# Kernel tuning notes

Hardware: AMD Instinct MI355X
Metric: run time of the kernel (lower is better)

## Reference

```python
import jax, jax.numpy as jnp
import numpy as np

B, S, E = 2, 2048, 2048
NH, NKV, HD = 32, 8, 64
GS = NH // NKV  # group size = 4
EPS = 1e-6
ROPE_THETA = 10000.0


def setup_inputs() -> dict:
    key = jax.random.key(0)
    ks = jax.random.split(key, 6)
    x = jax.random.normal(ks[0], (B, S, E), jnp.float32)
    position_ids = jnp.broadcast_to(jnp.arange(S, dtype=jnp.int32), (B, S))
    # causal additive mask [1,1,S,S]
    causal = jnp.tril(jnp.ones((S, S), jnp.bool_))
    attn_mask = jnp.where(causal, 0.0, -1e9).astype(jnp.float32)[None, None]
    sc = 0.02
    Wq = jax.random.normal(ks[1], (E, NH * HD), jnp.float32) * sc
    Wk = jax.random.normal(ks[2], (E, NKV * HD), jnp.float32) * sc
    Wv = jax.random.normal(ks[3], (E, NKV * HD), jnp.float32) * sc
    Wo = jax.random.normal(ks[4], (NH * HD, E), jnp.float32) * sc
    q_norm_w = jnp.ones((HD,), jnp.float32)
    k_norm_w = jnp.ones((HD,), jnp.float32)
    return {"x": x, "position_ids": position_ids, "attn_mask": attn_mask,
            "Wq": Wq, "Wk": Wk, "Wv": Wv, "Wo": Wo,
            "q_norm_w": q_norm_w, "k_norm_w": k_norm_w}


def rms_norm(x, w):
    dt = x.dtype
    xf = x.astype(jnp.float32)
    xf = xf * jax.lax.rsqrt(jnp.mean(xf * xf, axis=-1, keepdims=True) + EPS)
    return w * xf.astype(dt)


def apply_rope(x, position_ids):
    # x: [B, H, S, D]; rotate-half RoPE
    D = x.shape[-1]
    inv_freq = 1.0 / (ROPE_THETA ** (jnp.arange(0, D, 2, dtype=jnp.float32) / D))
    freqs = position_ids.astype(jnp.float32)[:, :, None] * inv_freq  # [B,S,D/2]
    cos = jnp.cos(freqs)[:, None]  # [B,1,S,D/2]
    sin = jnp.sin(freqs)[:, None]
    x1, x2 = x[..., : D // 2], x[..., D // 2 :]
    return jnp.concatenate([x1 * cos - x2 * sin, x2 * cos + x1 * sin], axis=-1).astype(x.dtype)


def reference(x, position_ids, attn_mask, Wq, Wk, Wv, Wo, q_norm_w, k_norm_w):
    b, s, _ = x.shape
    Q = (x @ Wq).reshape(b, s, NH, HD).transpose(0, 2, 1, 3)   # [B,NH,S,D]
    K = (x @ Wk).reshape(b, s, NKV, HD).transpose(0, 2, 1, 3)  # [B,NKV,S,D]
    V = (x @ Wv).reshape(b, s, NKV, HD).transpose(0, 2, 1, 3)
    Q = rms_norm(Q, q_norm_w)
    K = rms_norm(K, k_norm_w)
    Q = apply_rope(Q, position_ids)
    K = apply_rope(K, position_ids)
    new_kv_cache = (K, V)
    # GQA: head h attends with kv group h // GS == reshape heads -> (NKV, GS)
    Qg = Q.reshape(b, NKV, GS, s, HD)
    scores = jnp.einsum('bgqsd,bgtd->bgqst', Qg, K) / np.float32(np.sqrt(HD))
    scores = scores + attn_mask[:, :, None]  # broadcast over group dim
    attn = jax.nn.softmax(scores.astype(jnp.float32), axis=-1).astype(x.dtype)
    ctx = jnp.einsum('bgqst,bgtd->bgqsd', attn, V)             # [B,NKV,GS,S,D]
    ctx = ctx.reshape(b, NH, s, HD).transpose(0, 2, 1, 3).reshape(b, s, NH * HD)
    output = ctx @ Wo
    return output, new_kv_cache
```

## Files before the change

kernel.cpp:

```cpp
#include <hip/hip_runtime.h>
#include <stdint.h>

#define S_LEN 2048
#define EMB 2048
#define NHEADS 32
#define NKVH 8
#define HDIM 64

typedef float f32x4 __attribute__((ext_vector_type(4)));
typedef float f32x16 __attribute__((ext_vector_type(16)));
typedef __bf16 bf16x8 __attribute__((ext_vector_type(8)));
typedef unsigned int u32x4 __attribute__((ext_vector_type(4)));

typedef const __attribute__((address_space(1))) void* as1cv;
typedef __attribute__((address_space(3))) void* as3v;

__device__ __forceinline__ void gload_lds16(const void* g, void* l) {
  as1cv gp = (as1cv)(uintptr_t)g;
  as3v lp = (as3v)(uintptr_t)l;
  __builtin_amdgcn_global_load_lds(gp, lp, 16, 0, 0);
}

__device__ __forceinline__ unsigned cvt_pk_bf16(float lo, float hi) {
  unsigned r;
  asm("v_cvt_pk_bf16_f32 %0, %1, %2" : "=v"(r) : "v"(lo), "v"(hi));
  return r;
}

__device__ __forceinline__ void permswap(unsigned& a, unsigned& b) {
  asm("v_permlane32_swap_b32 %0, %1" : "+v"(a), "+v"(b));
}

__device__ __forceinline__ bf16x8 pack4(unsigned a, unsigned b, unsigned c, unsigned d) {
  union { u32x4 u; bf16x8 f; } x;
  x.u = (u32x4){a, b, c, d};
  return x.f;
}

__global__ void rope_table_kernel(float* __restrict__ cosT, float* __restrict__ sinT) {
  int p = blockIdx.x;
  int i = threadIdx.x;
  if (i < 32) {
    float inv = powf(10000.0f, -(float)i / 32.0f);
    float ang = (float)p * inv;
    cosT[p * 32 + i] = cosf(ang);
    sinT[p * 32 + i] = sinf(ang);
  }
}

__global__ __launch_bounds__(256) void prep_kernel(const float* __restrict__ x,
                                                   __bf16* __restrict__ xb,
                                                   const float* __restrict__ Wq,
                                                   const float* __restrict__ Wk,
                                                   const float* __restrict__ Wv,
                                                   const float* __restrict__ Wo,
                                                   __bf16* __restrict__ Wcat,
                                                   __bf16* __restrict__ Wot) {
  int bid = blockIdx.x;
  int tid = threadIdx.x;
  if (bid < 4096) {
    int i = bid * 256 + tid;
    f32x4 a = *(const f32x4*)(x + (size_t)i * 8);
    f32x4 b = *(const f32x4*)(x + (size_t)i * 8 + 4);
    bf16x8 o;
    o[0] = (__bf16)a[0]; o[1] = (__bf16)a[1]; o[2] = (__bf16)a[2]; o[3] = (__bf16)a[3];
    o[4] = (__bf16)b[0]; o[5] = (__bf16)b[1]; o[6] = (__bf16)b[2]; o[7] = (__bf16)b[3];
    *(bf16x8*)(xb + (size_t)i * 8) = o;
    return;
  }
  int lb = bid - 4096;
  const float* in;
  __bf16* out;
  int C, bx, by;
  if (lb < 1024) {
    in = Wq; out = Wcat; C = 2048; bx = lb & 31; by = lb >> 5;
  } else if (lb < 1280) {
    lb -= 1024;
    in = Wk; out = Wcat + (size_t)2048 * 2048; C = 512; bx = lb & 7; by = lb >> 3;
  } else if (lb < 1536) {
    lb -= 1280;
    in = Wv; out = Wcat + (size_t)2560 * 2048; C = 512; bx = lb & 7; by = lb >> 3;
  } else {
    lb -= 1536;
    in = Wo; out = Wot; C = 2048; bx = lb & 31; by = lb >> 5;
  }
  const int R = 2048;
  __shared__ float t[64][65];
  int c0 = bx * 64, r0 = by * 64;
#pragma unroll
  for (int i = 0; i < 16; ++i) {
    int e = i * 256 + tid;
    int rr = e >> 6, cc = e & 63;
    t[rr][cc] = in[(size_t)(r0 + rr) * C + c0 + cc];
  }
  __syncthreads();
#pragma unroll
  for (int i = 0; i < 16; ++i) {
    int e = i * 256 + tid;
    int rr = e >> 6, cc = e & 63;
    out[(size_t)(c0 + rr) * R + r0 + cc] = (__bf16)t[cc][rr];
  }
}

template <int BM, int BN, typename OUT>
__global__ __launch_bounds__(256, 2) void gemm4w_kernel(const __bf16* __restrict__ A,
                                                        const __bf16* __restrict__ B,
                                                        OUT* __restrict__ C,
                                                        int M, int N, int K) {
  constexpr int MF = (BM / 2) / 16;
  constexpr int NF = (BN / 2) / 16;
  constexpr int ROWS = BM + BN;
  constexpr int NCALL = ROWS / 32;
  constexpr int CHA = BM / 32;
  __shared__ __align__(16) __bf16 sm[2][ROWS * 64];

  const int NT = K >> 6;
  const int nt = N / BN;
  const int nwg = (M / BM) * nt;
  const int q8 = nwg >> 3;
  int wg = blockIdx.x;
  int swz = (wg & 7) * q8 + (wg >> 3);
  int bm = swz / nt, bn = swz % nt;
  size_t m0 = (size_t)bm * BM, n0 = (size_t)bn * BN;

  int tid = threadIdx.x;
  int L = tid & 63, w = tid >> 6;
  int wrow = w >> 1, wcol = w & 1;
  int l15 = L & 15, hi2 = L >> 4;
  int lx = (l15 & 7) << 4;
  const int cx0 = (hi2 << 4) ^ lx;
  const int cx1 = (64 + (hi2 << 4)) ^ lx;

  int srow = tid >> 3;
  int scol = ((tid & 7) ^ (srow & 7)) << 3;
  const __bf16* pA = A + (size_t)(m0 + srow) * K + scol;
  const __bf16* pB = B + (size_t)(n0 + srow) * K + scol;

  char* smb = (char*)sm;
  const int aRow = (wrow * (BM / 2) + l15) * 128;
  const int bRow = (BM + wcol * (BN / 2) + l15) * 128;

  f32x4 acc[MF][NF];
#pragma unroll
  for (int m = 0; m < MF; ++m)
#pragma unroll
    for (int n = 0; n < NF; ++n) acc[m][n] = (f32x4){0.f, 0.f, 0.f, 0.f};

  auto STG = [&](int buf, int c, int t) {
    const __bf16* s = (c < CHA) ? pA + (size_t)(c << 5) * K + ((size_t)t << 6)
                                : pB + (size_t)((c - CHA) << 5) * K + ((size_t)t << 6);
    gload_lds16(s, smb + buf * (ROWS * 128) + c * 4096 + tid * 16);
  };

#pragma unroll
  for (int c = 0; c < NCALL; ++c) STG(0, c, 0);
#pragma unroll
  for (int c = 0; c < NCALL; ++c) STG(1, c, 1);
  if constexpr (NCALL == 10) asm volatile("s_waitcnt vmcnt(10)" ::: "memory");
  else asm volatile("s_waitcnt vmcnt(8)" ::: "memory");
  __builtin_amdgcn_s_barrier();

  for (int t = 0; t < NT; ++t) {
    const char* aC = smb + (t & 1) * (ROWS * 128);
    bf16x8 af[MF][2], bf[NF][2];
#pragma unroll
    for (int n = 0; n < NF; ++n) {
      bf[n][0] = *(const bf16x8*)(aC + bRow + n * 2048 + cx0);
      bf[n][1] = *(const bf16x8*)(aC + bRow + n * 2048 + cx1);
    }
#pragma unroll
    for (int m = 0; m < MF; ++m) {
      af[m][0] = *(const bf16x8*)(aC + aRow + m * 2048 + cx0);
      af[m][1] = *(const bf16x8*)(aC + aRow + m * 2048 + cx1);
    }
    asm volatile("s_waitcnt lgkmcnt(4)" ::: "memory");
    __builtin_amdgcn_sched_barrier(0);
    __builtin_amdgcn_s_setprio(1);
#pragma unroll
    for (int m = 0; m < MF / 2; ++m)
#pragma unroll
      for (int n = 0; n < NF; ++n)
#pragma unroll
        for (int kk = 0; kk < 2; ++kk)
          acc[m][n] = __builtin_amdgcn_mfma_f32_16x16x32_bf16(
              kk ? af[m][1] : af[m][0], kk ? bf[n][1] : bf[n][0], acc[m][n], 0, 0, 0);
    __builtin_amdgcn_s_setprio(0);
    asm volatile("s_waitcnt lgkmcnt(0)" ::: "memory");
    __builtin_amdgcn_sched_barrier(0);
    __builtin_amdgcn_s_barrier();
    if (t + 2 < NT) {
#pragma unroll
      for (int c = 0; c < NCALL; ++c) STG(t & 1, c, t + 2);
    }
    __builtin_amdgcn_s_setprio(1);
#pragma unroll
    for (int m = MF / 2; m < MF; ++m)
#pragma unroll
      for (int n = 0; n < NF; ++n)
#pragma unroll
        for (int kk = 0; kk < 2; ++kk)
          acc[m][n] = __builtin_amdgcn_mfma_f32_16x16x32_bf16(
              kk ? af[m][1] : af[m][0], kk ? bf[n][1] : bf[n][0], acc[m][n], 0, 0, 0);
    __builtin_amdgcn_s_setprio(0);
    if (t + 2 < NT) {
      if constexpr (NCALL == 10) asm volatile("s_waitcnt vmcnt(10)" ::: "memory");
      else asm volatile("s_waitcnt vmcnt(8)" ::: "memory");
    } else if (t + 1 < NT) {
      asm volatile("s_waitcnt vmcnt(0)" ::: "memory");
    }
    __builtin_amdgcn_s_barrier();
  }

#pragma unroll
  for (int m = 0; m < MF; ++m)
#pragma unroll
    for (int n = 0; n < NF; ++n)
#pragma unroll
      for (int r = 0; r < 4; ++r)
        C[(m0 + wrow * (BM / 2) + m * 16 + (hi2 << 2) + r) * (size_t)N + n0 +
          wcol * (BN / 2) + n * 16 + l15] = (OUT)acc[m][n][r];
}

__global__ __launch_bounds__(256) void rmsrope_kernel(
    const __bf16* __restrict__ QKV, const int* __restrict__ pos,
    const float* __restrict__ qw, const float* __restrict__ kw,
    const float* __restrict__ cosT, const float* __restrict__ sinT,
    __bf16* __restrict__ Qatt, __bf16* __restrict__ Katt, __bf16* __restrict__ Vtatt,
    float* __restrict__ Kc, float* __restrict__ Vc) {
  int token = blockIdx.x;
  int b = token >> 11, s = token & 2047;
  int tid = threadIdx.x, lane = tid & 63, wid = tid >> 6;
  int p = pos[token];
  int i = lane & 31;
  float cs = cosT[p * 32 + i], sn = sinT[p * 32 + i];
  const __bf16* base = QKV + (size_t)token * 3072;
  float qwl = qw[lane], kwl = kw[lane];
  const float qscale = 0.18033688011112042f;

  for (int h = wid; h < NHEADS; h += 4) {
    float v = (float)base[h * 64 + lane];
    float ss = v * v;
#pragma unroll
    for (int m = 1; m < 64; m <<= 1) ss += __shfl_xor(ss, m);
    float xn = v * rsqrtf(ss * (1.0f / 64.0f) + 1e-6f) * qwl;
    float other = __shfl_xor(xn, 32);
    float o = xn * cs + ((lane < 32) ? -other * sn : other * sn);
    Qatt[((size_t)(b * NHEADS + h) * S_LEN + s) * HDIM + lane] = (__bf16)(o * qscale);
  }
  for (int g = wid; g < NKVH; g += 4) {
    float v = (float)base[2048 + g * 64 + lane];
    float ss = v * v;
#pragma unroll
    for (int m = 1; m < 64; m <<= 1) ss += __shfl_xor(ss, m);
    float xn = v * rsqrtf(ss * (1.0f / 64.0f) + 1e-6f) * kwl;
    float other = __shfl_xor(xn, 32);
    float o = xn * cs + ((lane < 32) ? -other * sn : other * sn);
    size_t kidx = ((size_t)(b * NKVH + g) * S_LEN + s) * HDIM + lane;
    Katt[kidx] = (__bf16)o;
    Kc[kidx] = o;
  }
  for (int g = wid; g < NKVH; g += 4) {
    float v = (float)base[2560 + g * 64 + lane];
    size_t vidx = ((size_t)(b * NKVH + g) * S_LEN + s) * HDIM + lane;
    Vc[vidx] = v;
    Vtatt[((size_t)(b * NKVH + g) * HDIM + lane) * S_LEN + s] = (__bf16)v;
  }
}

__global__ __launch_bounds__(256, 2) void attn_kernel(const __bf16* __restrict__ Qatt,
                                                      const __bf16* __restrict__ Katt,
                                                      const __bf16* __restrict__ Vtatt,
                                                      __bf16* __restrict__ ctx) {
  __shared__ __align__(16) __bf16 Ks[2][4096];
  __shared__ __align__(16) __bf16 Vs[2][4096];
  int bid = blockIdx.x;
  int qt, bg;
  if (bid < 256) { qt = 31 - (bid >> 4); bg = bid & 15; }
  else { qt = (bid - 256) >> 4; bg = bid & 15; }
  int b = bg >> 3, g = bg & 7;
  int tid = threadIdx.x, lane = tid & 63, w = tid >> 6;
  int l31 = lane & 31, hi = lane >> 5;
  int h = g * 4 + w;

  const __bf16* Kg = Katt + (size_t)bg * (S_LEN * HDIM);
  const __bf16* Vg = Vtatt + (size_t)bg * (HDIM * S_LEN);
  const __bf16* Qg = Qatt + ((size_t)(b * NHEADS + h) * S_LEN + qt * 64 + l31) * HDIM;

  bf16x8 qf0[4], qf1[4];
#pragma unroll
  for (int ds = 0; ds < 4; ++ds) {
    qf0[ds] = *(const bf16x8*)(Qg + ds * 16 + (hi << 3));
    qf1[ds] = *(const bf16x8*)(Qg + 32 * HDIM + ds * 16 + (hi << 3));
  }

  f32x16 acc00, acc01, acc10, acc11;
#pragma unroll
  for (int r = 0; r < 16; ++r) { acc00[r] = 0.f; acc01[r] = 0.f; acc10[r] = 0.f; acc11[r] = 0.f; }
  float l0 = 0.f, l1 = 0.f;

  int sr = tid >> 3;
  int sc = ((tid & 7) ^ (sr & 7)) << 3;
  const __bf16* Ksrc = Kg + (size_t)sr * HDIM + sc;
  const __bf16* Vsrc = Vg + (size_t)sr * S_LEN + sc;

  gload_lds16(Ksrc, &Ks[0][tid * 8]);
  gload_lds16(Ksrc + 32 * HDIM, &Ks[0][2048 + tid * 8]);
  gload_lds16(Vsrc, &Vs[0][tid * 8]);
  gload_lds16(Vsrc + (size_t)32 * S_LEN, &Vs[0][2048 + tid * 8]);
  __syncthreads();

  int rx = (l31 & 7) << 4;

  for (int t = 0; t <= qt; ++t) {
    int cur = t & 1;
    if (t < qt) {
      const __bf16* kn = Ksrc + (size_t)(t + 1) * (64 * HDIM);
      const __bf16* vn = Vsrc + (size_t)(t + 1) * 64;
      gload_lds16(kn, &Ks[cur ^ 1][tid * 8]);
      gload_lds16(kn + 32 * HDIM, &Ks[cur ^ 1][2048 + tid * 8]);
      gload_lds16(vn, &Vs[cur ^ 1][tid * 8]);
      gload_lds16(vn + (size_t)32 * S_LEN, &Vs[cur ^ 1][2048 + tid * 8]);
    }
    f32x16 s00, s01, s10, s11;
#pragma unroll
    for (int r = 0; r < 16; ++r) { s00[r] = 0.f; s01[r] = 0.f; s10[r] = 0.f; s11[r] = 0.f; }
    {
      const char* kb0 = (const char*)Ks[cur] + (size_t)l31 * 128;
      const char* kb1 = kb0 + 4096;
#pragma unroll
      for (int dstep = 0; dstep < 4; ++dstep) {
        int cb = dstep * 32 + (hi << 4);
        bf16x8 k0 = *(const bf16x8*)(kb0 + (cb ^ rx));
        bf16x8 k1 = *(const bf16x8*)(kb1 + (cb ^ rx));
        s00 = __builtin_amdgcn_mfma_f32_32x32x16_bf16(k0, qf0[dstep], s00, 0, 0, 0);
        s01 = __builtin_amdgcn_mfma_f32_32x32x16_bf16(k1, qf0[dstep], s01, 0, 0, 0);
        s10 = __builtin_amdgcn_mfma_f32_32x32x16_bf16(k0, qf1[dstep], s10, 0, 0, 0);
        s11 = __builtin_amdgcn_mfma_f32_32x32x16_bf16(k1, qf1[dstep], s11, 0, 0, 0);
      }
    }
    if (t == qt) {
#pragma unroll
      for (int r = 0; r < 16; ++r) {
        int kb = (r & 3) + 8 * (r >> 2) + (hi << 2);
        if (kb > l31) { s00[r] = -3e38f; s11[r] = -3e38f; }
        s01[r] = -3e38f;
      }
    }
#pragma unroll
    for (int r = 0; r < 16; ++r) {
      s00[r] = __builtin_amdgcn_exp2f(s00[r]);
      s01[r] = __builtin_amdgcn_exp2f(s01[r]);
      s10[r] = __builtin_amdgcn_exp2f(s10[r]);
      s11[r] = __builtin_amdgcn_exp2f(s11[r]);
    }
    {
      float a0 = 0.f, a1 = 0.f, a2 = 0.f, a3 = 0.f;
      float b0 = 0.f, b1 = 0.f, b2 = 0.f, b3 = 0.f;
#pragma unroll
      for (int r = 0; r < 16; r += 4) {
        a0 += s00[r]; a1 += s00[r + 1]; a2 += s00[r + 2]; a3 += s00[r + 3];
        a0 += s01[r]; a1 += s01[r + 1]; a2 += s01[r + 2]; a3 += s01[r + 3];
        b0 += s10[r]; b1 += s10[r + 1]; b2 += s10[r + 2]; b3 += s10[r + 3];
        b0 += s11[r]; b1 += s11[r + 1]; b2 += s11[r + 2]; b3 += s11[r + 3];
      }
      l0 += (a0 + a1) + (a2 + a3);
      l1 += (b0 + b1) + (b2 + b3);
    }
    bf16x8 pf0[4], pf1[4];
    {
      unsigned wd[8];
#pragma unroll
      for (int i = 0; i < 8; ++i) wd[i] = cvt_pk_bf16(s00[2 * i], s00[2 * i + 1]);
      permswap(wd[0], wd[2]); permswap(wd[1], wd[3]);
      permswap(wd[4], wd[6]); permswap(wd[5], wd[7]);
      pf0[0] = pack4(wd[0], wd[1], wd[2], wd[3]);
      pf0[1] = pack4(wd[4], wd[5], wd[6], wd[7]);
#pragma unroll
      for (int i = 0; i < 8; ++i) wd[i] = cvt_pk_bf16(s01[2 * i], s01[2 * i + 1]);
      permswap(wd[0], wd[2]); permswap(wd[1], wd[3]);
      permswap(wd[4], wd[6]); permswap(wd[5], wd[7]);
      pf0[2] = pack4(wd[0], wd[1], wd[2], wd[3]);
      pf0[3] = pack4(wd[4], wd[5], wd[6], wd[7]);
#pragma unroll
      for (int i = 0; i < 8; ++i) wd[i] = cvt_pk_bf16(s10[2 * i], s10[2 * i + 1]);
      permswap(wd[0], wd[2]); permswap(wd[1], wd[3]);
      permswap(wd[4], wd[6]); permswap(wd[5], wd[7]);
      pf1[0] = pack4(wd[0], wd[1], wd[2], wd[3]);
      pf1[1] = pack4(wd[4], wd[5], wd[6], wd[7]);
#pragma unroll
      for (int i = 0; i < 8; ++i) wd[i] = cvt_pk_bf16(s11[2 * i], s11[2 * i + 1]);
      permswap(wd[0], wd[2]); permswap(wd[1], wd[3]);
      permswap(wd[4], wd[6]); permswap(wd[5], wd[7]);
      pf1[2] = pack4(wd[0], wd[1], wd[2], wd[3]);
      pf1[3] = pack4(wd[4], wd[5], wd[6], wd[7]);
    }
    {
      const char* vb0 = (const char*)Vs[cur] + (size_t)l31 * 128;
      const char* vb1 = vb0 + 4096;
#pragma unroll
      for (int ks = 0; ks < 4; ++ks) {
        int cb = ks * 32 + (hi << 4);
        bf16x8 v0 = *(const bf16x8*)(vb0 + (cb ^ rx));
        bf16x8 v1 = *(const bf16x8*)(vb1 + (cb ^ rx));
        acc00 = __builtin_amdgcn_mfma_f32_32x32x16_bf16(v0, pf0[ks], acc00, 0, 0, 0);
        acc01 = __builtin_amdgcn_mfma_f32_32x32x16_bf16(v1, pf0[ks], acc01, 0, 0, 0);
        acc10 = __builtin_amdgcn_mfma_f32_32x32x16_bf16(v0, pf1[ks], acc10, 0, 0, 0);
        acc11 = __builtin_amdgcn_mfma_f32_32x32x16_bf16(v1, pf1[ks], acc11, 0, 0, 0);
      }
    }
    __syncthreads();
  }

  l0 += __shfl_xor(l0, 32);
  l1 += __shfl_xor(l1, 32);
  float inv0 = 1.f / l0, inv1 = 1.f / l1;
  size_t orow0 = ((size_t)(b * S_LEN + qt * 64 + l31)) * EMB + h * HDIM;
  size_t orow1 = orow0 + (size_t)32 * EMB;
#pragma unroll
  for (int r = 0; r < 16; r += 2) {
    int d = (r & 3) + 8 * (r >> 2) + (hi << 2);
    unsigned w00 = cvt_pk_bf16(acc00[r] * inv0, acc00[r + 1] * inv0);
    unsigned w01 = cvt_pk_bf16(acc01[r] * inv0, acc01[r + 1] * inv0);
    unsigned w10 = cvt_pk_bf16(acc10[r] * inv1, acc10[r + 1] * inv1);
    unsigned w11 = cvt_pk_bf16(acc11[r] * inv1, acc11[r + 1] * inv1);
    *(unsigned*)((char*)ctx + (orow0 + d) * 2) = w00;
    *(unsigned*)((char*)ctx + (orow0 + 32 + d) * 2) = w01;
    *(unsigned*)((char*)ctx + (orow1 + d) * 2) = w10;
    *(unsigned*)((char*)ctx + (orow1 + 32 + d) * 2) = w11;
  }
}

extern "C" void kernel_launch(void* const* d_in, const int* in_sizes, int n_in,
                              void* d_out, int out_size, void* d_ws, size_t ws_size,
                              hipStream_t stream) {
  const float* x = (const float*)d_in[0];
  const int* pos = (const int*)d_in[1];
  const float* Wq = (const float*)d_in[3];
  const float* Wk = (const float*)d_in[4];
  const float* Wv = (const float*)d_in[5];
  const float* Wo = (const float*)d_in[6];
  const float* qw = (const float*)d_in[7];
  const float* kw = (const float*)d_in[8];

  float* out = (float*)d_out;
  float* Kc = out + (size_t)2 * 2048 * 2048;
  float* Vc = Kc + (size_t)2 * 8 * 2048 * 64;

  char* ws = (char*)d_ws;
  size_t off = 0;
  auto alloc = [&](size_t bytes) {
    char* p = ws + off;
    off += (bytes + 255) & ~(size_t)255;
    return (void*)p;
  };
  __bf16* xb = (__bf16*)alloc((size_t)4096 * 2048 * 2);
  __bf16* Wcat = (__bf16*)alloc((size_t)3072 * 2048 * 2);
  __bf16* Wot = (__bf16*)alloc((size_t)2048 * 2048 * 2);
  __bf16* QKV = (__bf16*)alloc((size_t)4096 * 3072 * 2);
  __bf16* ctx = (__bf16*)alloc((size_t)4096 * 2048 * 2);
  __bf16* Qatt = (__bf16*)alloc((size_t)2 * 32 * 2048 * 64 * 2);
  __bf16* Katt = (__bf16*)alloc((size_t)2 * 8 * 2048 * 64 * 2);
  __bf16* Vtat = (__bf16*)alloc((size_t)2 * 8 * 2048 * 64 * 2);
  float* cosT = (float*)alloc((size_t)2048 * 32 * 4);
  float* sinT = (float*)alloc((size_t)2048 * 32 * 4);

  rope_table_kernel<<<2048, 64, 0, stream>>>(cosT, sinT);
  prep_kernel<<<6656, 256, 0, stream>>>(x, xb, Wq, Wk, Wv, Wo, Wcat, Wot);
  gemm4w_kernel<128, 192, __bf16><<<512, 256, 0, stream>>>(xb, Wcat, QKV, 4096, 3072, 2048);
  rmsrope_kernel<<<4096, 256, 0, stream>>>(QKV, pos, qw, kw, cosT, sinT, Qatt, Katt, Vtat, Kc, Vc);
  attn_kernel<<<512, 256, 0, stream>>>(Qatt, Katt, Vtat, ctx);
  gemm4w_kernel<128, 128, float><<<512, 256, 0, stream>>>(ctx, Wot, out, 4096, 2048, 2048);
}
```

Before: 179.8 us.

## Fuse Q RMSNorm+RoPE into attention prologue and merge rope table into prep

Moves the per-head Q RMSNorm, RoPE and scaling out of the separate norm kernel and into the attention kernel prologue. Each lane now reads its Q row slice straight from the QKV buffer, normalizes and rotates it in registers, and packs it to bf16 MFMA operands. This removes the Qatt intermediate write and read and leaves the standalone kernel handling only K and V. The rope cos/sin table build is also folded into prep_kernel as extra blocks, saving one launch, at the cost of more register pressure in the attention kernel.

```diff
diff --git a/kernel.cpp b/kernel.cpp
--- a/kernel.cpp
+++ b/kernel.cpp
@@ -35,17 +35,6 @@
   union { u32x4 u; bf16x8 f; } x;
   x.u = (u32x4){a, b, c, d};
   return x.f;
-}
-
-__global__ void rope_table_kernel(float* __restrict__ cosT, float* __restrict__ sinT) {
-  int p = blockIdx.x;
-  int i = threadIdx.x;
-  if (i < 32) {
-    float inv = powf(10000.0f, -(float)i / 32.0f);
-    float ang = (float)p * inv;
-    cosT[p * 32 + i] = cosf(ang);
-    sinT[p * 32 + i] = sinf(ang);
-  }
 }
 
 __global__ __launch_bounds__(256) void prep_kernel(const float* __restrict__ x,
@@ -55,7 +44,9 @@
                                                    const float* __restrict__ Wv,
                                                    const float* __restrict__ Wo,
                                                    __bf16* __restrict__ Wcat,
-                                                   __bf16* __restrict__ Wot) {
+                                                   __bf16* __restrict__ Wot,
+                                                   float* __restrict__ cosT,
+                                                   float* __restrict__ sinT) {
   int bid = blockIdx.x;
   int tid = threadIdx.x;
   if (bid < 4096) {
@@ -66,6 +57,17 @@
     o[0] = (__bf16)a[0]; o[1] = (__bf16)a[1]; o[2] = (__bf16)a[2]; o[3] = (__bf16)a[3];
     o[4] = (__bf16)b[0]; o[5] = (__bf16)b[1]; o[6] = (__bf16)b[2]; o[7] = (__bf16)b[3];
     *(bf16x8*)(xb + (size_t)i * 8) = o;
+    return;
+  }
+  if (bid >= 6656) {
+    int p = (bid - 6656) * 4 + (tid >> 6);
+    int i = tid & 63;
+    if (i < 32) {
+      float inv = powf(10000.0f, -(float)i / 32.0f);
+      float ang = (float)p * inv;
+      cosT[p * 32 + i] = cosf(ang);
+      sinT[p * 32 + i] = sinf(ang);
+    }
     return;
   }
   int lb = bid - 4096;
@@ -221,11 +223,11 @@
           wcol * (BN / 2) + n * 16 + l15] = (OUT)acc[m][n][r];
 }
 
-__global__ __launch_bounds__(256) void rmsrope_kernel(
+__global__ __launch_bounds__(256) void kvrope_kernel(
     const __bf16* __restrict__ QKV, const int* __restrict__ pos,
-    const float* __restrict__ qw, const float* __restrict__ kw,
+    const float* __restrict__ kw,
     const float* __restrict__ cosT, const float* __restrict__ sinT,
-    __bf16* __restrict__ Qatt, __bf16* __restrict__ Katt, __bf16* __restrict__ Vtatt,
+    __bf16* __restrict__ Katt, __bf16* __restrict__ Vtatt,
     float* __restrict__ Kc, float* __restrict__ Vc) {
   int token = blockIdx.x;
   int b = token >> 11, s = token & 2047;
@@ -234,19 +236,8 @@
   int i = lane & 31;
   float cs = cosT[p * 32 + i], sn = sinT[p * 32 + i];
   const __bf16* base = QKV + (size_t)token * 3072;
-  float qwl = qw[lane], kwl = kw[lane];
-  const float qscale = 0.18033688011112042f;
-
-  for (int h = wid; h < NHEADS; h += 4) {
-    float v = (float)base[h * 64 + lane];
-    float ss = v * v;
-#pragma unroll
-    for (int m = 1; m < 64; m <<= 1) ss += __shfl_xor(ss, m);
-    float xn = v * rsqrtf(ss * (1.0f / 64.0f) + 1e-6f) * qwl;
-    float other = __shfl_xor(xn, 32);
-    float o = xn * cs + ((lane < 32) ? -other * sn : other * sn);
-    Qatt[((size_t)(b * NHEADS + h) * S_LEN + s) * HDIM + lane] = (__bf16)(o * qscale);
-  }
+  float kwl = kw[lane];
+
   for (int g = wid; g < NKVH; g += 4) {
     float v = (float)base[2048 + g * 64 + lane];
     float ss = v * v;
@@ -267,7 +258,11 @@
   }
 }
 
-__global__ __launch_bounds__(256, 2) void attn_kernel(const __bf16* __restrict__ Qatt,
+__global__ __launch_bounds__(256, 2) void attn_kernel(const __bf16* __restrict__ QKV,
+                                                      const int* __restrict__ pos,
+                                                      const float* __restrict__ qw,
+                                                      const float* __restrict__ cosT,
+                                                      const float* __restrict__ sinT,
                                                       const __bf16* __restrict__ Katt,
                                                       const __bf16* __restrict__ Vtatt,
                                                       __bf16* __restrict__ ctx) {
@@ -284,13 +279,56 @@
 
   const __bf16* Kg = Katt + (size_t)bg * (S_LEN * HDIM);
   const __bf16* Vg = Vtatt + (size_t)bg * (HDIM * S_LEN);
-  const __bf16* Qg = Qatt + ((size_t)(b * NHEADS + h) * S_LEN + qt * 64 + l31) * HDIM;
-
-  bf16x8 qf0[4], qf1[4];
+
+  const float qscale = 0.18033688011112042f;
+  float qwf[4][8];
 #pragma unroll
   for (int ds = 0; ds < 4; ++ds) {
-    qf0[ds] = *(const bf16x8*)(Qg + ds * 16 + (hi << 3));
-    qf1[ds] = *(const bf16x8*)(Qg + 32 * HDIM + ds * 16 + (hi << 3));
+    *(f32x4*)&qwf[ds][0] = *(const f32x4*)(qw + ds * 16 + (hi << 3));
+    *(f32x4*)&qwf[ds][4] = *(const f32x4*)(qw + ds * 16 + (hi << 3) + 4);
+  }
+  bf16x8 qf[2][4];
+#pragma unroll
+  for (int qs = 0; qs < 2; ++qs) {
+    int row = qt * 64 + qs * 32 + l31;
+    const __bf16* qr = QKV + ((size_t)(b * S_LEN + row)) * 3072 + h * 64;
+    float v[4][8];
+    float ss = 0.f;
+#pragma unroll
+    for (int ds = 0; ds < 4; ++ds) {
+      bf16x8 a = *(const bf16x8*)(qr + ds * 16 + (hi << 3));
+#pragma unroll
+      for (int j = 0; j < 8; ++j) {
+        v[ds][j] = (float)a[j];
+        ss += v[ds][j] * v[ds][j];
+      }
+    }
+    ss += __shfl_xor(ss, 32);
+    float rr = rsqrtf(ss * (1.0f / 64.0f) + 1e-6f) * qscale;
+    int p = pos[b * S_LEN + row];
+    const float* cb = cosT + p * 32 + (hi << 3);
+    const float* sb = sinT + p * 32 + (hi << 3);
+    float cl[8], ch[8], sl[8], sh[8];
+    *(f32x4*)&cl[0] = *(const f32x4*)cb;        *(f32x4*)&cl[4] = *(const f32x4*)(cb + 4);
+    *(f32x4*)&ch[0] = *(const f32x4*)(cb + 16); *(f32x4*)&ch[4] = *(const f32x4*)(cb + 20);
+    *(f32x4*)&sl[0] = *(const f32x4*)sb;        *(f32x4*)&sl[4] = *(const f32x4*)(sb + 4);
+    *(f32x4*)&sh[0] = *(const f32x4*)(sb + 16); *(f32x4*)&sh[4] = *(const f32x4*)(sb + 20);
+    float o[4][8];
+#pragma unroll
+    for (int j = 0; j < 8; ++j) {
+      float x0 = v[0][j] * rr * qwf[0][j];
+      float x1 = v[1][j] * rr * qwf[1][j];
+      float x2 = v[2][j] * rr * qwf[2][j];
+      float x3 = v[3][j] * rr * qwf[3][j];
+      o[0][j] = x0 * cl[j] - x2 * sl[j];
+      o[1][j] = x1 * ch[j] - x3 * sh[j];
+      o[2][j] = x2 * cl[j] + x0 * sl[j];
+      o[3][j] = x3 * ch[j] + x1 * sh[j];
+    }
+#pragma unroll
+    for (int ds = 0; ds < 4; ++ds)
+      qf[qs][ds] = pack4(cvt_pk_bf16(o[ds][0], o[ds][1]), cvt_pk_bf16(o[ds][2], o[ds][3]),
+                         cvt_pk_bf16(o[ds][4], o[ds][5]), cvt_pk_bf16(o[ds][6], o[ds][7]));
   }
 
   f32x16 acc00, acc01, acc10, acc11;
@@ -332,10 +370,10 @@
         int cb = dstep * 32 + (hi << 4);
         bf16x8 k0 = *(const bf16x8*)(kb0 + (cb ^ rx));
         bf16x8 k1 = *(const bf16x8*)(kb1 + (cb ^ rx));
-        s00 = __builtin_amdgcn_mfma_f32_32x32x16_bf16(k0, qf0[dstep], s00, 0, 0, 0);
-        s01 = __builtin_amdgcn_mfma_f32_32x32x16_bf16(k1, qf0[dstep], s01, 0, 0, 0);
-        s10 = __builtin_amdgcn_mfma_f32_32x32x16_bf16(k0, qf1[dstep], s10, 0, 0, 0);
-        s11 = __builtin_amdgcn_mfma_f32_32x32x16_bf16(k1, qf1[dstep], s11, 0, 0, 0);
+        s00 = __builtin_amdgcn_mfma_f32_32x32x16_bf16(k0, qf[0][dstep], s00, 0, 0, 0);
+        s01 = __builtin_amdgcn_mfma_f32_32x32x16_bf16(k1, qf[0][dstep], s01, 0, 0, 0);
+        s10 = __builtin_amdgcn_mfma_f32_32x32x16_bf16(k0, qf[1][dstep], s10, 0, 0, 0);
+        s11 = __builtin_amdgcn_mfma_f32_32x32x16_bf16(k1, qf[1][dstep], s11, 0, 0, 0);
       }
     }
     if (t == qt) {
@@ -458,16 +496,14 @@
   __bf16* Wot = (__bf16*)alloc((size_t)2048 * 2048 * 2);
   __bf16* QKV = (__bf16*)alloc((size_t)4096 * 3072 * 2);
   __bf16* ctx = (__bf16*)alloc((size_t)4096 * 2048 * 2);
-  __bf16* Qatt = (__bf16*)alloc((size_t)2 * 32 * 2048 * 64 * 2);
   __bf16* Katt = (__bf16*)alloc((size_t)2 * 8 * 2048 * 64 * 2);
   __bf16* Vtat = (__bf16*)alloc((size_t)2 * 8 * 2048 * 64 * 2);
   float* cosT = (float*)alloc((size_t)2048 * 32 * 4);
   float* sinT = (float*)alloc((size_t)2048 * 32 * 4);
 
-  rope_table_kernel<<<2048, 64, 0, stream>>>(cosT, sinT);
-  prep_kernel<<<6656, 256, 0, stream>>>(x, xb, Wq, Wk, Wv, Wo, Wcat, Wot);
+  prep_kernel<<<7168, 256, 0, stream>>>(x, xb, Wq, Wk, Wv, Wo, Wcat, Wot, cosT, sinT);
   gemm4w_kernel<128, 192, __bf16><<<512, 256, 0, stream>>>(xb, Wcat, QKV, 4096, 3072, 2048);
-  rmsrope_kernel<<<4096, 256, 0, stream>>>(QKV, pos, qw, kw, cosT, sinT, Qatt, Katt, Vtat, Kc, Vc);
-  attn_kernel<<<512, 256, 0, stream>>>(Qatt, Katt, Vtat, ctx);
+  kvrope_kernel<<<4096, 256, 0, stream>>>(QKV, pos, kw, cosT, sinT, Katt, Vtat, Kc, Vc);
+  attn_kernel<<<512, 256, 0, stream>>>(QKV, pos, qw, cosT, sinT, Katt, Vtat, ctx);
   gemm4w_kernel<128, 128, float><<<512, 256, 0, stream>>>(ctx, Wot, out, 4096, 2048, 2048);
 }
```

Result: faster. 169.2 us (-5.9%).
